# Kernel optimization log

Hardware: AMD Instinct MI355X
Metric: run time of the kernel (lower is better)

Reference implementation:

```python
import jax, jax.numpy as jnp
import numpy as np

N = 80000
E = 1280000
C_IN, HID, C_OUT = 3, 64, 1
DEPTH = 3
KS = [40000, 20000, 10000]  # ceil(0.5 * n) per pooling level
EPS = 1e-5


def gcn_conv(x, W, src, dst, ew, n, fill=2.0):
    # PyG GCNConv with add_self_loops=True; improved => self-loop weight fill=2.0
    h = x @ W                                           # [n, F]
    deg = jax.ops.segment_sum(ew, dst, num_segments=n) + fill
    dinv = jax.lax.rsqrt(deg)
    norm = dinv[src] * ew * dinv[dst]                   # [E]
    agg = jax.ops.segment_sum(norm[:, None] * h[src], dst, num_segments=n)
    return agg + (fill * dinv * dinv)[:, None] * h      # self-loop term


def batchnorm(x, gamma, beta):
    # BatchNorm1d in training mode: biased batch stats over the node dim
    mu = jnp.mean(x, axis=0)
    var = jnp.var(x, axis=0)
    return gamma * (x - mu) * jax.lax.rsqrt(var + EPS) + beta


def gcn_block(x, src, dst, ew, n, W, gamma, beta, fill=2.0):
    return jax.nn.relu(batchnorm(gcn_conv(x, W, src, dst, ew, n, fill), gamma, beta))


def topk_pool(x, src, dst, ew, w, k):
    # TopKPooling with ReLU nonlinearity: score = relu(x.w / ||w||)
    n = x.shape[0]
    score = jax.nn.relu(x @ w / jnp.linalg.norm(w))
    sc, perm = jax.lax.top_k(score, k)
    xk = x[perm] * sc[:, None]
    # filter_adj with fixed edge count: invalid edges get weight 0 (no-op in GCN)
    mapping = jnp.full((n,), -1, dtype=src.dtype).at[perm].set(
        jnp.arange(k, dtype=src.dtype))
    ns, nd = mapping[src], mapping[dst]
    valid = (ns >= 0) & (nd >= 0)
    ns = jnp.where(valid, ns, 0)
    nd = jnp.where(valid, nd, 0)
    new_ew = jnp.where(valid, ew, jnp.zeros((), ew.dtype))
    return xk, ns, nd, new_ew, perm


def _forward(x, edge_index, Wd, gd, bd, pw, Wu, gu, bu, W_out):
    src, dst = edge_index[0], edge_index[1]
    ew = jnp.ones(src.shape, x.dtype)
    n = x.shape[0]
    x = gcn_block(x, src, dst, ew, n, Wd[0], gd[0], bd[0])
    xs, sds, ews, perms = [x], [(src, dst)], [ew], []
    for i in range(DEPTH):
        x, src, dst, ew, perm = topk_pool(x, src, dst, ew, pw[i], KS[i])
        x = gcn_block(x, src, dst, ew, KS[i], Wd[i + 1], gd[i + 1], bd[i + 1])
        if i < DEPTH - 1:
            xs.append(x); sds.append((src, dst)); ews.append(ew)
        perms.append(perm)
    for i in range(DEPTH):
        j = DEPTH - 1 - i
        res = xs[j]; src, dst = sds[j]; ew = ews[j]; perm = perms[j]
        up = jnp.zeros_like(res).at[perm].set(x)
        x = res + up
        if i < DEPTH - 1:
            x = gcn_block(x, src, dst, ew, res.shape[0], Wu[i], gu[i], bu[i])
        else:
            x = jax.nn.sigmoid(
                gcn_conv(x, W_out, src, dst, ew, res.shape[0], fill=1.0))
    return x


def setup_inputs() -> dict:
    key = jax.random.key(0)
    ks = jax.random.split(key, 16)
    nrm = lambda k, shape: jax.random.normal(k, shape, jnp.float32) * 0.1
    inp = {
        "x": jax.random.normal(ks[0], (N, C_IN), jnp.float32),
        "edge_index": jax.random.randint(ks[1], (2, E), 0, N, jnp.int32),
    }
    dims = [(C_IN, HID)] + [(HID, HID)] * DEPTH
    ki = 2
    for l, (a, b) in enumerate(dims):
        inp[f"W_d{l}"] = nrm(ks[ki], (a, b)); ki += 1
        inp[f"g_d{l}"] = jnp.ones((b,), jnp.float32)
        inp[f"b_d{l}"] = jnp.zeros((b,), jnp.float32)
    for l in range(DEPTH):
        inp[f"pw{l}"] = nrm(ks[ki], (HID,)); ki += 1
    for l in range(DEPTH - 1):
        inp[f"W_u{l}"] = nrm(ks[ki], (HID, HID)); ki += 1
        inp[f"g_u{l}"] = jnp.ones((HID,), jnp.float32)
        inp[f"b_u{l}"] = jnp.zeros((HID,), jnp.float32)
    inp["W_out"] = nrm(ks[ki], (HID, C_OUT))
    return inp


def reference(x, edge_index, W_d0, g_d0, b_d0, W_d1, g_d1, b_d1, W_d2, g_d2,
              b_d2, W_d3, g_d3, b_d3, pw0, pw1, pw2, W_u0, g_u0, b_u0,
              W_u1, g_u1, b_u1, W_out):
    Wd = [W_d0, W_d1, W_d2, W_d3]
    gd = [g_d0, g_d1, g_d2, g_d3]
    bd = [b_d0, b_d1, b_d2, b_d3]
    pw = [pw0, pw1, pw2]
    Wu = [W_u0, W_u1]
    gu = [g_u0, g_u1]
    bu = [b_u0, b_u1]
    return _forward(x, edge_index, Wd, gd, bd, pw, Wu, gu, bu, W_out)
```

## Files before the change

kernel.cpp:

```cpp
#include <hip/hip_runtime.h>
#include <cstdint>
#include <utility>

#define NN0 80000
#define NE 1280000
#define MMB_GRID 1024

static inline int cdiv(int a, int b){ return (a+b-1)/b; }

__global__ void k_matmul_bn(const float* __restrict__ x, const float* __restrict__ W,
                            float* __restrict__ h, float* __restrict__ part, int n){
  __shared__ float ls[64], lq[64];
  int f = threadIdx.x & 63;
  float sa = 0.f, sq = 0.f;
  int total = n*64, stride = gridDim.x*blockDim.x;
  for (int t = blockIdx.x*blockDim.x + threadIdx.x; t < total; t += stride){
    int i = t >> 6;
    const float* xr = x + i*64;
    const float* wc = W + f;
    float s = 0.f;
    #pragma unroll
    for (int k2 = 0; k2 < 64; k2++) s += xr[k2]*wc[k2*64];
    h[t] = s; sa += s; sq += s*s;
  }
  if (threadIdx.x < 64){ ls[threadIdx.x] = 0.f; lq[threadIdx.x] = 0.f; }
  __syncthreads();
  atomicAdd(&ls[f], sa); atomicAdd(&lq[f], sq);
  __syncthreads();
  if (threadIdx.x < 128)
    part[blockIdx.x*128 + threadIdx.x] =
      (threadIdx.x < 64) ? ls[threadIdx.x] : lq[threadIdx.x-64];
}

__global__ void k_matmul_bn3(const float* __restrict__ x, const float* __restrict__ W,
                             float* __restrict__ h, float* __restrict__ part, int n){
  __shared__ float ls[64], lq[64];
  int f = threadIdx.x & 63;
  float sa = 0.f, sq = 0.f;
  int total = n*64, stride = gridDim.x*blockDim.x;
  for (int t = blockIdx.x*blockDim.x + threadIdx.x; t < total; t += stride){
    int i = t >> 6;
    float s = x[i*3]*W[f] + x[i*3+1]*W[64+f] + x[i*3+2]*W[128+f];
    h[t] = s; sa += s; sq += s*s;
  }
  if (threadIdx.x < 64){ ls[threadIdx.x] = 0.f; lq[threadIdx.x] = 0.f; }
  __syncthreads();
  atomicAdd(&ls[f], sa); atomicAdd(&lq[f], sq);
  __syncthreads();
  if (threadIdx.x < 128)
    part[blockIdx.x*128 + threadIdx.x] =
      (threadIdx.x < 64) ? ls[threadIdx.x] : lq[threadIdx.x-64];
}

__global__ void k_stats_reduce(const float* __restrict__ part, float* __restrict__ stats){
  int c = blockIdx.x, lane = threadIdx.x;
  float s = 0.f;
  for (int b = lane; b < MMB_GRID; b += 64) s += part[b*128 + c];
  for (int o = 32; o > 0; o >>= 1) s += __shfl_xor(s, o);
  if (lane == 0) stats[c] = s;
}

__global__ void k_matvec(const float* __restrict__ x, const float* __restrict__ W,
                         float* __restrict__ h1, int n){
  int lane = threadIdx.x & 63, w = threadIdx.x >> 6;
  int wid = blockIdx.x*4 + w, nw = gridDim.x*4;
  float wv = W[lane];
  for (int i = wid; i < n; i += nw){
    float v = x[i*64+lane]*wv;
    for (int o = 32; o > 0; o >>= 1) v += __shfl_xor(v, o);
    if (lane == 0) h1[i] = v;
  }
}

__global__ void k_zero_i(int* __restrict__ p, int n){
  int t = blockIdx.x*blockDim.x + threadIdx.x;
  if (t < n) p[t] = 0;
}

__global__ void k_scan_part(const int* __restrict__ in, int* __restrict__ bsum, int n){
  __shared__ int ws[256];
  int base = blockIdx.x*1024 + threadIdx.x*4;
  int s = 0;
  #pragma unroll
  for (int u = 0; u < 4; u++){ int i = base+u; if (i < n) s += in[i]; }
  ws[threadIdx.x] = s; __syncthreads();
  for (int st = 128; st > 0; st >>= 1){
    if (threadIdx.x < st) ws[threadIdx.x] += ws[threadIdx.x+st];
    __syncthreads();
  }
  if (threadIdx.x == 0) bsum[blockIdx.x] = ws[0];
}

__global__ void k_scan_fin_rp(const int* __restrict__ in, const int* __restrict__ bsum, int nb,
                              int* __restrict__ rp, int* __restrict__ cursor, int n){
  __shared__ int bws[256]; __shared__ int ws[256];
  int t = threadIdx.x;
  bws[t] = (t < nb) ? bsum[t] : 0; __syncthreads();
  for (int st = 1; st < 256; st <<= 1){
    int a = (t >= st) ? bws[t-st] : 0; __syncthreads();
    bws[t] += a; __syncthreads();
  }
  int blockoff = (blockIdx.x == 0) ? 0 : bws[blockIdx.x-1];
  int base = blockIdx.x*1024 + t*4;
  int v[4]; int s = 0;
  #pragma unroll
  for (int u = 0; u < 4; u++){ int i = base+u; v[u] = (i < n) ? in[i] : 0; s += v[u]; }
  ws[t] = s; __syncthreads();
  for (int st = 1; st < 256; st <<= 1){
    int a = (t >= st) ? ws[t-st] : 0; __syncthreads();
    ws[t] += a; __syncthreads();
  }
  int off = blockoff + ws[t] - s;
  #pragma unroll
  for (int u = 0; u < 4; u++){
    int i = base+u;
    if (i < n){
      rp[i] = off; cursor[i] = off; off += v[u];
      if (i == n-1) rp[n] = off;
    }
  }
}

__global__ void k_hist_full(const int* __restrict__ dst, int* __restrict__ indeg, int ne){
  int e = blockIdx.x*blockDim.x + threadIdx.x;
  if (e < ne) atomicAdd(&indeg[dst[e]], 1);
}
__global__ void k_scatter_full(const int* __restrict__ src, const int* __restrict__ dst,
                               int* __restrict__ cursor, int* __restrict__ col, int ne){
  int e = blockIdx.x*blockDim.x + threadIdx.x;
  if (e >= ne) return;
  int pos = atomicAdd(&cursor[dst[e]], 1);
  col[pos] = src[e];
}

__global__ void k_hist_mapped(const int* __restrict__ rp_p, const int* __restrict__ col_p,
                              const int* __restrict__ mapv, int* __restrict__ indeg, int np){
  int d = blockIdx.x*blockDim.x + threadIdx.x;
  if (d >= np) return;
  int md = mapv[d];
  if (md < 0) return;
  int c = 0, e = rp_p[d+1];
  for (int j = rp_p[d]; j < e; j++) if (mapv[col_p[j]] >= 0) c++;
  indeg[md] = c;
}
__global__ void k_scatter_mapped(const int* __restrict__ rp_p, const int* __restrict__ col_p,
                                 const int* __restrict__ mapv, const int* __restrict__ rp_c,
                                 int* __restrict__ col_c, int np){
  int d = blockIdx.x*blockDim.x + threadIdx.x;
  if (d >= np) return;
  int md = mapv[d];
  if (md < 0) return;
  int pos = rp_c[md], e = rp_p[d+1];
  for (int j = rp_p[d]; j < e; j++){
    int ms = mapv[col_p[j]];
    if (ms >= 0) col_c[pos++] = ms;
  }
}

__global__ void k_dinv_rp(const int* __restrict__ rp, float* __restrict__ dinv,
                          float fill, int n){
  int i = blockIdx.x*blockDim.x + threadIdx.x;
  if (i < n) dinv[i] = 1.0f/sqrtf((float)(rp[i+1]-rp[i]) + fill);
}

__global__ void k_gather64(const int* __restrict__ rp, const int* __restrict__ col,
                           const float* __restrict__ dinv, const float* __restrict__ x,
                           float* __restrict__ y, int n){
  int t = blockIdx.x*blockDim.x + threadIdx.x;
  int i = t >> 6, f = t & 63;
  if (i >= n) return;
  int beg = rp[i], end = rp[i+1];
  float di = dinv[i];
  float acc = 0.f;
  for (int j = beg; j < end; j++){
    int s = col[j];
    acc += dinv[s]*x[s*64+f];
  }
  y[i*64+f] = di*acc + 2.f*di*di*x[i*64+f];
}

__global__ void k_gather3(const int* __restrict__ rp, const int* __restrict__ col,
                          const float* __restrict__ dinv, const float* __restrict__ x,
                          float* __restrict__ y, int n){
  int i = blockIdx.x*blockDim.x + threadIdx.x;
  if (i >= n) return;
  int beg = rp[i], end = rp[i+1];
  float di = dinv[i];
  float a0 = 0.f, a1 = 0.f, a2 = 0.f;
  for (int j = beg; j < end; j++){
    int s = col[j];
    float ds = dinv[s];
    a0 += ds*x[s*3+0]; a1 += ds*x[s*3+1]; a2 += ds*x[s*3+2];
  }
  float sl = 2.f*di*di;
  y[i*3+0] = di*a0 + sl*x[i*3+0];
  y[i*3+1] = di*a1 + sl*x[i*3+1];
  y[i*3+2] = di*a2 + sl*x[i*3+2];
}

__global__ void k_gather_sig(const int* __restrict__ rp, const int* __restrict__ col,
                             const float* __restrict__ dinv, const float* __restrict__ h1,
                             float* __restrict__ out, int n){
  int i = blockIdx.x*blockDim.x + threadIdx.x;
  if (i >= n) return;
  int beg = rp[i], end = rp[i+1];
  float di = dinv[i];
  float acc = 0.f;
  for (int j = beg; j < end; j++) acc += dinv[col[j]]*h1[col[j]];
  float v = di*acc + di*di*h1[i];
  out[i] = 1.f/(1.f+expf(-v));
}

__global__ void k_bnrelu(float* __restrict__ x, const float* __restrict__ stats,
                         const float* __restrict__ gamma, const float* __restrict__ beta,
                         int n) {
  int t = blockIdx.x*blockDim.x + threadIdx.x;
  if (t >= n*64) return;
  int f = t & 63;
  float inv_n = 1.0f/(float)n;
  float mu = stats[f]*inv_n;
  float var = stats[64+f]*inv_n - mu*mu;
  float v = gamma[f]*(x[t]-mu)*(1.0f/sqrtf(var+1e-5f)) + beta[f];
  x[t] = fmaxf(v, 0.f);
}

__global__ void k_bnrelu_score(float* __restrict__ x, const float* __restrict__ stats,
                               const float* __restrict__ gamma, const float* __restrict__ beta,
                               const float* __restrict__ pw,
                               float* __restrict__ score, unsigned* __restrict__ key,
                               int* __restrict__ idx, int n, int P){
  int lane = threadIdx.x & 63, w = threadIdx.x >> 6;
  int wid = blockIdx.x*4 + w, nw = gridDim.x*4;
  float inv_n = 1.f/(float)n;
  float mu = stats[lane]*inv_n;
  float var = stats[64+lane]*inv_n - mu*mu;
  float gs = gamma[lane]*(1.f/sqrtf(var+1e-5f));
  float bt = beta[lane];
  float pv = pw[lane];
  float q = pv*pv;
  for (int o = 32; o > 0; o >>= 1) q += __shfl_xor(q, o);
  float qn = 1.f/sqrtf(q);
  for (int i = wid; i < n; i += nw){
    float v = fmaxf(gs*(x[i*64+lane]-mu)+bt, 0.f);
    x[i*64+lane] = v;
    float s = v*pv;
    for (int o = 32; o > 0; o >>= 1) s += __shfl_xor(s, o);
    if (lane == 0){
      float sc = fmaxf(s*qn, 0.f);
      score[i] = sc; key[i] = ~__float_as_uint(sc); idx[i] = i;
    }
  }
  for (int g = n + wid; g < P; g += nw)
    if (lane == 0){ key[g] = 0xFFFFFFFFu; idx[g] = 0; }
}

__global__ void k_radix_hist(const unsigned* __restrict__ key, int* __restrict__ hist,
                             int shift, int nblk){
  __shared__ int lh[256];
  lh[threadIdx.x] = 0; __syncthreads();
  int base = blockIdx.x*1024 + threadIdx.x;
  #pragma unroll
  for (int u = 0; u < 4; u++){
    unsigned d = (key[base + u*256] >> shift) & 255u;
    atomicAdd(&lh[d], 1);
  }
  __syncthreads();
  hist[threadIdx.x*nblk + blockIdx.x] = lh[threadIdx.x];
}

__global__ void k_radix_scatter(const unsigned* __restrict__ keyin, const int* __restrict__ idxin,
                                unsigned* __restrict__ keyout, int* __restrict__ idxout,
                                const int* __restrict__ hist, int shift, int nblk){
  __shared__ int dbase[256], run[256], sc[256];
  __shared__ int wcnt[4][256];
  int t = threadIdx.x, lane = t & 63, w = t >> 6;
  int pre = 0, tot = 0;
  for (int b = 0; b < nblk; b++){
    int v = hist[t*nblk + b];
    if (b < blockIdx.x) pre += v;
    tot += v;
  }
  sc[t] = tot; __syncthreads();
  for (int st = 1; st < 256; st <<= 1){
    int a = (t >= st) ? sc[t-st] : 0; __syncthreads();
    sc[t] += a; __syncthreads();
  }
  dbase[t] = sc[t] - tot + pre;
  run[t] = 0;
  for (int u = 0; u < 4; u++){
    wcnt[0][t] = 0; wcnt[1][t] = 0; wcnt[2][t] = 0; wcnt[3][t] = 0;
    __syncthreads();
    int g = blockIdx.x*1024 + u*256 + t;
    unsigned kk = keyin[g]; int id = idxin[g];
    unsigned d = (kk >> shift) & 255u;
    unsigned long long m = ~0ull;
    #pragma unroll
    for (int b = 0; b < 8; b++){
      unsigned long long bal = __ballot((d >> b) & 1u);
      m &= ((d >> b) & 1u) ? bal : ~bal;
    }
    int rnk = __popcll(m & ((1ull << lane) - 1ull));
    if (rnk == 0) wcnt[w][d] = __popcll(m);
    __syncthreads();
    int off2 = run[d] + rnk;
    for (int w2 = 0; w2 < w; w2++) off2 += wcnt[w2][d];
    int pos = dbase[d] + off2;
    keyout[pos] = kk; idxout[pos] = id;
    __syncthreads();
    run[t] += wcnt[0][t] + wcnt[1][t] + wcnt[2][t] + wcnt[3][t];
    __syncthreads();
  }
}

__global__ void k_select_sorted(const int* __restrict__ idxs, int* __restrict__ perm,
                                int* __restrict__ mapping, int n, int k){
  int r = blockIdx.x*blockDim.x + threadIdx.x;
  if (r >= n) return;
  int i = idxs[r];
  mapping[i] = (r < k) ? r : -1;
  if (r < k) perm[r] = i;
}

__global__ void k_gather_scale(const float* __restrict__ x, const float* __restrict__ score,
                               const int* __restrict__ perm, float* __restrict__ xk, int k) {
  int t = blockIdx.x*blockDim.x + threadIdx.x;
  if (t >= k*64) return;
  int r = t >> 6, f = t & 63;
  int i = perm[r];
  xk[t] = x[i*64+f]*score[i];
}

__global__ void k_scatter_add(const float* __restrict__ xup, const int* __restrict__ perm,
                              float* __restrict__ res, int k) {
  int t = blockIdx.x*blockDim.x + threadIdx.x;
  if (t >= k*64) return;
  int r = t >> 6, f = t & 63;
  res[perm[r]*64+f] += xup[t];
}

extern "C" void kernel_launch(void* const* d_in, const int* in_sizes, int n_in,
                              void* d_out, int out_size, void* d_ws, size_t ws_size,
                              hipStream_t stream) {
  const float* x_in = (const float*)d_in[0];
  const int* ei = (const int*)d_in[1];
  const int* src0 = ei;
  const int* dst0 = ei + NE;
  const float* W_d[4] = {(const float*)d_in[2],(const float*)d_in[5],(const float*)d_in[8],(const float*)d_in[11]};
  const float* g_d[4] = {(const float*)d_in[3],(const float*)d_in[6],(const float*)d_in[9],(const float*)d_in[12]};
  const float* b_d[4] = {(const float*)d_in[4],(const float*)d_in[7],(const float*)d_in[10],(const float*)d_in[13]};
  const float* pw[3]  = {(const float*)d_in[14],(const float*)d_in[15],(const float*)d_in[16]};
  const float* W_u[2] = {(const float*)d_in[17],(const float*)d_in[20]};
  const float* g_u[2] = {(const float*)d_in[18],(const float*)d_in[21]};
  const float* b_u[2] = {(const float*)d_in[19],(const float*)d_in[22]};
  const float* W_out  = (const float*)d_in[23];
  float* out = (float*)d_out;

  float* base = (float*)d_ws;
  size_t off = 0;
  auto alloc = [&](size_t nf){ float* p = base + off; off += nf; return p; };
  float* x0 = alloc(5120000);
  float* x1 = alloc(2560000);
  float* x2 = alloc(1280000);
  float* x3 = alloc(640000);
  float* A  = alloc(2560000);
  float* h  = alloc(5120000);
  int* col0 = (int*)alloc(NE);
  int* col1 = (int*)alloc(NE);
  int* col2 = (int*)alloc(NE);
  int* col3 = (int*)alloc(NE);
  int* rp0 = (int*)alloc(80001);
  int* rp1 = (int*)alloc(40001);
  int* rp2 = (int*)alloc(20001);
  int* rp3 = (int*)alloc(10001);
  int* indeg  = (int*)alloc(NN0);
  int* cursor = (int*)alloc(NN0);
  float* dinv0  = alloc(NN0);
  float* dinv0f = alloc(NN0);
  float* dinv1  = alloc(40000);
  float* dinv2  = alloc(20000);
  float* dinv3  = alloc(10000);
  float* score = alloc(NN0);
  int* mapv = (int*)alloc(NN0);
  int* p0 = (int*)alloc(40000);
  int* p1 = (int*)alloc(20000);
  int* p2 = (int*)alloc(10000);
  float* stats = alloc(128);
  float* part  = alloc(MMB_GRID*128);
  unsigned* keyA = (unsigned*)alloc(81920);
  unsigned* keyB = (unsigned*)alloc(81920);
  int* idxA = (int*)alloc(81920);
  int* idxB = (int*)alloc(81920);
  int* hist = (int*)alloc(81920);
  int* bsum = (int*)alloc(256);
  (void)ws_size; (void)in_sizes; (void)n_in; (void)out_size;

  const int B = 256;

  auto scan_csr = [&](const int* indeg_, int* rp, int* cur, int n2){
    int nb = cdiv(n2, 1024);
    k_scan_part  <<<nb, 256, 0, stream>>>(indeg_, bsum, n2);
    k_scan_fin_rp<<<nb, 256, 0, stream>>>(indeg_, bsum, nb, rp, cur, n2);
  };

  auto conv = [&](const float* xin, int Fin, const float* W, int n,
                  const int* rp, const int* col, const float* dv, float* dstb){
    if (Fin == 3){
      k_gather3   <<<cdiv(n,B), B, 0, stream>>>(rp, col, dv, xin, h, n);
      k_matmul_bn3<<<MMB_GRID, B, 0, stream>>>(h, W, dstb, part, n);
    } else {
      k_gather64  <<<cdiv(n*64,B), B, 0, stream>>>(rp, col, dv, xin, h, n);
      k_matmul_bn <<<MMB_GRID, B, 0, stream>>>(h, W, dstb, part, n);
    }
    k_stats_reduce<<<128, 64, 0, stream>>>(part, stats);
  };

  auto pool = [&](float* xb, const float* g, const float* bt, const float* w,
                  int n, int k, int* pm, float* xk){
    int nblk = cdiv(n, 1024), P = nblk*1024;
    k_bnrelu_score<<<512, B, 0, stream>>>(xb, stats, g, bt, w, score, keyA, idxA, n, P);
    unsigned* ka = keyA; int* ia = idxA; unsigned* kb = keyB; int* ib = idxB;
    for (int pass = 0; pass < 4; pass++){
      k_radix_hist   <<<nblk, 256, 0, stream>>>(ka, hist, pass*8, nblk);
      k_radix_scatter<<<nblk, 256, 0, stream>>>(ka, ia, kb, ib, hist, pass*8, nblk);
      std::swap(ka, kb); std::swap(ia, ib);
    }
    k_select_sorted<<<cdiv(n,B), B, 0, stream>>>(ia, pm, mapv, n, k);
    k_gather_scale <<<cdiv(k*64,B), B, 0, stream>>>(xb, score, pm, xk, k);
  };

  auto csr_mapped = [&](const int* rp_p, const int* col_p, int np, int nc,
                        int* rp_c, int* col_c, float* dv){
    k_hist_mapped<<<cdiv(np,B), B, 0, stream>>>(rp_p, col_p, mapv, indeg, np);
    scan_csr(indeg, rp_c, cursor, nc);
    k_scatter_mapped<<<cdiv(np,B), B, 0, stream>>>(rp_p, col_p, mapv, rp_c, col_c, np);
    k_dinv_rp<<<cdiv(nc,B), B, 0, stream>>>(rp_c, dv, 2.f, nc);
  };

  k_zero_i   <<<cdiv(NN0,B), B, 0, stream>>>(indeg, NN0);
  k_hist_full<<<cdiv(NE,B),  B, 0, stream>>>(dst0, indeg, NE);
  scan_csr(indeg, rp0, cursor, NN0);
  k_scatter_full<<<cdiv(NE,B), B, 0, stream>>>(src0, dst0, cursor, col0, NE);
  k_dinv_rp<<<cdiv(NN0,B), B, 0, stream>>>(rp0, dinv0,  2.f, NN0);
  k_dinv_rp<<<cdiv(NN0,B), B, 0, stream>>>(rp0, dinv0f, 1.f, NN0);

  conv(x_in, 3, W_d[0], NN0, rp0, col0, dinv0, x0);
  pool(x0, g_d[0], b_d[0], pw[0], NN0, 40000, p0, A);
  csr_mapped(rp0, col0, NN0, 40000, rp1, col1, dinv1);

  conv(A, 64, W_d[1], 40000, rp1, col1, dinv1, x1);
  pool(x1, g_d[1], b_d[1], pw[1], 40000, 20000, p1, A);
  csr_mapped(rp1, col1, 40000, 20000, rp2, col2, dinv2);

  conv(A, 64, W_d[2], 20000, rp2, col2, dinv2, x2);
  pool(x2, g_d[2], b_d[2], pw[2], 20000, 10000, p2, A);
  csr_mapped(rp2, col2, 20000, 10000, rp3, col3, dinv3);

  conv(A, 64, W_d[3], 10000, rp3, col3, dinv3, x3);
  k_bnrelu<<<cdiv(10000*64,B), B, 0, stream>>>(x3, stats, g_d[3], b_d[3], 10000);

  k_scatter_add<<<cdiv(10000*64,B), B, 0, stream>>>(x3, p2, x2, 10000);
  conv(x2, 64, W_u[0], 20000, rp2, col2, dinv2, A);
  k_bnrelu<<<cdiv(20000*64,B), B, 0, stream>>>(A, stats, g_u[0], b_u[0], 20000);

  k_scatter_add<<<cdiv(20000*64,B), B, 0, stream>>>(A, p1, x1, 20000);
  conv(x1, 64, W_u[1], 40000, rp1, col1, dinv1, A);
  k_bnrelu<<<cdiv(40000*64,B), B, 0, stream>>>(A, stats, g_u[1], b_u[1], 40000);

  k_scatter_add<<<cdiv(40000*64,B), B, 0, stream>>>(A, p0, x0, 40000);

  float* h1 = score;
  k_matvec<<<512, B, 0, stream>>>(x0, W_out, h1, NN0);
  k_gather_sig<<<cdiv(NN0,B), B, 0, stream>>>(rp0, col0, dinv0f, h1, out, NN0);
}
```

Baseline: 899.8 us.

## Build level-0 CSR via stable 3-pass radix sort of edges by destination

Replaces the atomic histogram plus atomic-cursor scatter for the initial CSR with a three-pass 6-bit LSD radix sort of (dst, src) pairs, followed by a binary search per node to find row pointers and both dinv arrays. It also folds dinv computation into the scan kernel for pooled levels and fuses select and gather-scale into one kernel. The aim is to avoid contended global atomics and to produce sorted, deterministic column order that gathers better. In exchange it adds nine extra launches and several full passes over 1.28M edges, plus extra workspace.

```diff
diff --git a/kernel.cpp b/kernel.cpp
--- a/kernel.cpp
+++ b/kernel.cpp
@@ -5,6 +5,8 @@
 #define NN0 80000
 #define NE 1280000
 #define MMB_GRID 1024
+#define EB 2048
+#define ENB 625
 
 static inline int cdiv(int a, int b){ return (a+b-1)/b; }
 
@@ -72,9 +74,65 @@
   }
 }
 
-__global__ void k_zero_i(int* __restrict__ p, int n){
-  int t = blockIdx.x*blockDim.x + threadIdx.x;
-  if (t < n) p[t] = 0;
+__global__ void k_ehist6(const int* __restrict__ key, int* __restrict__ hist, int shift){
+  __shared__ int lh[64];
+  if (threadIdx.x < 64) lh[threadIdx.x] = 0;
+  __syncthreads();
+  int base = blockIdx.x*EB + threadIdx.x;
+  #pragma unroll
+  for (int u = 0; u < 8; u++)
+    atomicAdd(&lh[(key[base + u*256] >> shift) & 63], 1);
+  __syncthreads();
+  if (threadIdx.x < 64) hist[threadIdx.x*ENB + blockIdx.x] = lh[threadIdx.x];
+}
+
+__global__ void k_escatter6(const int* __restrict__ keyin, const int* __restrict__ valin,
+                            int* __restrict__ keyout, int* __restrict__ valout,
+                            const int* __restrict__ hist, int shift){
+  __shared__ int dbase[64], run[64], wcnt[4][64];
+  int t = threadIdx.x, lane = t & 63, w = t >> 6;
+  if (t < 64){ dbase[t] = hist[t*ENB + blockIdx.x]; run[t] = 0; }
+  __syncthreads();
+  for (int u = 0; u < 8; u++){
+    if (t < 64){ wcnt[0][t]=0; wcnt[1][t]=0; wcnt[2][t]=0; wcnt[3][t]=0; }
+    __syncthreads();
+    int g = blockIdx.x*EB + u*256 + t;
+    int kk = keyin[g], vv = valin[g];
+    int d = (kk >> shift) & 63;
+    unsigned long long m = ~0ull;
+    #pragma unroll
+    for (int b = 0; b < 6; b++){
+      unsigned long long bal = __ballot((d >> b) & 1);
+      m &= ((d >> b) & 1) ? bal : ~bal;
+    }
+    int rnk = __popcll(m & ((1ull << lane) - 1ull));
+    if (rnk == 0) wcnt[w][d] = __popcll(m);
+    __syncthreads();
+    int off2 = run[d] + rnk;
+    for (int w2 = 0; w2 < w; w2++) off2 += wcnt[w2][d];
+    int pos = dbase[d] + off2;
+    keyout[pos] = kk; valout[pos] = vv;
+    __syncthreads();
+    if (t < 64) run[t] += wcnt[0][t] + wcnt[1][t] + wcnt[2][t] + wcnt[3][t];
+    __syncthreads();
+  }
+}
+
+__global__ void k_rp_search(const int* __restrict__ skey, int* __restrict__ rp,
+                            float* __restrict__ dinvA, float* __restrict__ dinvB, int n){
+  int i = blockIdx.x*blockDim.x + threadIdx.x;
+  if (i >= n) return;
+  int lo = 0, hi = NE;
+  while (lo < hi){ int mid = (lo+hi)>>1; if (skey[mid] < i) lo = mid+1; else hi = mid; }
+  int a = lo;
+  lo = a; hi = NE;
+  while (lo < hi){ int mid = (lo+hi)>>1; if (skey[mid] < i+1) lo = mid+1; else hi = mid; }
+  int b2 = lo;
+  rp[i] = a;
+  if (i == n-1) rp[n] = NE;
+  float deg = (float)(b2 - a);
+  dinvA[i] = 1.0f/sqrtf(deg + 2.f);
+  dinvB[i] = 1.0f/sqrtf(deg + 1.f);
 }
 
 __global__ void k_scan_part(const int* __restrict__ in, int* __restrict__ bsum, int n){
@@ -92,7 +150,7 @@
 }
 
 __global__ void k_scan_fin_rp(const int* __restrict__ in, const int* __restrict__ bsum, int nb,
-                              int* __restrict__ rp, int* __restrict__ cursor, int n){
+                              int* __restrict__ rp, float* __restrict__ dinvA, int n){
   __shared__ int bws[256]; __shared__ int ws[256];
   int t = threadIdx.x;
   bws[t] = (t < nb) ? bsum[t] : 0; __syncthreads();
@@ -115,22 +173,37 @@
   for (int u = 0; u < 4; u++){
     int i = base+u;
     if (i < n){
-      rp[i] = off; cursor[i] = off; off += v[u];
+      rp[i] = off; off += v[u];
+      dinvA[i] = 1.0f/sqrtf((float)v[u] + 2.f);
       if (i == n-1) rp[n] = off;
     }
   }
 }
 
-__global__ void k_hist_full(const int* __restrict__ dst, int* __restrict__ indeg, int ne){
-  int e = blockIdx.x*blockDim.x + threadIdx.x;
-  if (e < ne) atomicAdd(&indeg[dst[e]], 1);
-}
-__global__ void k_scatter_full(const int* __restrict__ src, const int* __restrict__ dst,
-                               int* __restrict__ cursor, int* __restrict__ col, int ne){
-  int e = blockIdx.x*blockDim.x + threadIdx.x;
-  if (e >= ne) return;
-  int pos = atomicAdd(&cursor[dst[e]], 1);
-  col[pos] = src[e];
+__global__ void k_scan_fin_flat(int* __restrict__ data, const int* __restrict__ bsum, int nb, int n){
+  __shared__ int bws[256]; __shared__ int ws[256];
+  int t = threadIdx.x;
+  bws[t] = (t < nb) ? bsum[t] : 0; __syncthreads();
+  for (int st = 1; st < 256; st <<= 1){
+    int a = (t >= st) ? bws[t-st] : 0; __syncthreads();
+    bws[t] += a; __syncthreads();
+  }
+  int blockoff = (blockIdx.x == 0) ? 0 : bws[blockIdx.x-1];
+  int base = blockIdx.x*1024 + t*4;
+  int v[4]; int s = 0;
+  #pragma unroll
+  for (int u = 0; u < 4; u++){ int i = base+u; v[u] = (i < n) ? data[i] : 0; s += v[u]; }
+  ws[t] = s; __syncthreads();
+  for (int st = 1; st < 256; st <<= 1){
+    int a = (t >= st) ? ws[t-st] : 0; __syncthreads();
+    ws[t] += a; __syncthreads();
+  }
+  int off = blockoff + ws[t] - s;
+  #pragma unroll
+  for (int u = 0; u < 4; u++){
+    int i = base+u;
+    if (i < n){ data[i] = off; off += v[u]; }
+  }
 }
 
 __global__ void k_hist_mapped(const int* __restrict__ rp_p, const int* __restrict__ col_p,
@@ -155,12 +228,6 @@
     int ms = mapv[col_p[j]];
     if (ms >= 0) col_c[pos++] = ms;
   }
-}
-
-__global__ void k_dinv_rp(const int* __restrict__ rp, float* __restrict__ dinv,
-                          float fill, int n){
-  int i = blockIdx.x*blockDim.x + threadIdx.x;
-  if (i < n) dinv[i] = 1.0f/sqrtf((float)(rp[i+1]-rp[i]) + fill);
 }
 
 __global__ void k_gather64(const int* __restrict__ rp, const int* __restrict__ col,
@@ -312,22 +379,20 @@
   }
 }
 
-__global__ void k_select_sorted(const int* __restrict__ idxs, int* __restrict__ perm,
-                                int* __restrict__ mapping, int n, int k){
-  int r = blockIdx.x*blockDim.x + threadIdx.x;
-  if (r >= n) return;
-  int i = idxs[r];
-  mapping[i] = (r < k) ? r : -1;
-  if (r < k) perm[r] = i;
-}
-
-__global__ void k_gather_scale(const float* __restrict__ x, const float* __restrict__ score,
-                               const int* __restrict__ perm, float* __restrict__ xk, int k) {
+__global__ void k_select_gather(const int* __restrict__ idxs, const float* __restrict__ x,
+                                const float* __restrict__ score, int* __restrict__ perm,
+                                int* __restrict__ mapv, float* __restrict__ xk, int n, int k){
   int t = blockIdx.x*blockDim.x + threadIdx.x;
-  if (t >= k*64) return;
-  int r = t >> 6, f = t & 63;
-  int i = perm[r];
-  xk[t] = x[i*64+f]*score[i];
+  if (t < n){
+    int i = idxs[t];
+    mapv[i] = (t < k) ? t : -1;
+    if (t < k) perm[t] = i;
+  }
+  if (t < k*64){
+    int r = t >> 6, f = t & 63;
+    int i = idxs[r];
+    xk[t] = x[i*64+f]*score[i];
+  }
 }
 
 __global__ void k_scatter_add(const float* __restrict__ xup, const int* __restrict__ perm,
@@ -368,12 +433,15 @@
   int* col1 = (int*)alloc(NE);
   int* col2 = (int*)alloc(NE);
   int* col3 = (int*)alloc(NE);
+  int* ek1 = (int*)alloc(NE);
+  int* ev1 = (int*)alloc(NE);
+  int* ek2 = (int*)alloc(NE);
+  int* ev2 = (int*)alloc(NE);
   int* rp0 = (int*)alloc(80001);
   int* rp1 = (int*)alloc(40001);
   int* rp2 = (int*)alloc(20001);
   int* rp3 = (int*)alloc(10001);
   int* indeg  = (int*)alloc(NN0);
-  int* cursor = (int*)alloc(NN0);
   float* dinv0  = alloc(NN0);
   float* dinv0f = alloc(NN0);
   float* dinv1  = alloc(40000);
@@ -391,15 +459,21 @@
   int* idxA = (int*)alloc(81920);
   int* idxB = (int*)alloc(81920);
   int* hist = (int*)alloc(81920);
+  int* ehist = (int*)alloc(64*ENB);
   int* bsum = (int*)alloc(256);
   (void)ws_size; (void)in_sizes; (void)n_in; (void)out_size;
 
   const int B = 256;
 
-  auto scan_csr = [&](const int* indeg_, int* rp, int* cur, int n2){
+  auto scan_flat = [&](int* data, int n2){
+    int nb = cdiv(n2, 1024);
+    k_scan_part    <<<nb, 256, 0, stream>>>(data, bsum, n2);
+    k_scan_fin_flat<<<nb, 256, 0, stream>>>(data, bsum, nb, n2);
+  };
+  auto scan_csr = [&](const int* indeg_, int* rp, float* dv, int n2){
     int nb = cdiv(n2, 1024);
     k_scan_part  <<<nb, 256, 0, stream>>>(indeg_, bsum, n2);
-    k_scan_fin_rp<<<nb, 256, 0, stream>>>(indeg_, bsum, nb, rp, cur, n2);
+    k_scan_fin_rp<<<nb, 256, 0, stream>>>(indeg_, bsum, nb, rp, dv, n2);
   };
 
   auto conv = [&](const float* xin, int Fin, const float* W, int n,
@@ -424,24 +498,26 @@
       k_radix_scatter<<<nblk, 256, 0, stream>>>(ka, ia, kb, ib, hist, pass*8, nblk);
       std::swap(ka, kb); std::swap(ia, ib);
     }
-    k_select_sorted<<<cdiv(n,B), B, 0, stream>>>(ia, pm, mapv, n, k);
-    k_gather_scale <<<cdiv(k*64,B), B, 0, stream>>>(xb, score, pm, xk, k);
+    k_select_gather<<<cdiv(k*64,B), B, 0, stream>>>(ia, xb, score, pm, mapv, xk, n, k);
   };
 
   auto csr_mapped = [&](const int* rp_p, const int* col_p, int np, int nc,
                         int* rp_c, int* col_c, float* dv){
     k_hist_mapped<<<cdiv(np,B), B, 0, stream>>>(rp_p, col_p, mapv, indeg, np);
-    scan_csr(indeg, rp_c, cursor, nc);
+    scan_csr(indeg, rp_c, dv, nc);
     k_scatter_mapped<<<cdiv(np,B), B, 0, stream>>>(rp_p, col_p, mapv, rp_c, col_c, np);
-    k_dinv_rp<<<cdiv(nc,B), B, 0, stream>>>(rp_c, dv, 2.f, nc);
   };
 
-  k_zero_i   <<<cdiv(NN0,B), B, 0, stream>>>(indeg, NN0);
-  k_hist_full<<<cdiv(NE,B),  B, 0, stream>>>(dst0, indeg, NE);
-  scan_csr(indeg, rp0, cursor, NN0);
-  k_scatter_full<<<cdiv(NE,B), B, 0, stream>>>(src0, dst0, cursor, col0, NE);
-  k_dinv_rp<<<cdiv(NN0,B), B, 0, stream>>>(rp0, dinv0,  2.f, NN0);
-  k_dinv_rp<<<cdiv(NN0,B), B, 0, stream>>>(rp0, dinv0f, 1.f, NN0);
+  k_ehist6   <<<ENB, B, 0, stream>>>(dst0, ehist, 0);
+  scan_flat(ehist, 64*ENB);
+  k_escatter6<<<ENB, B, 0, stream>>>(dst0, src0, ek1, ev1, ehist, 0);
+  k_ehist6   <<<ENB, B, 0, stream>>>(ek1, ehist, 6);
+  scan_flat(ehist, 64*ENB);
+  k_escatter6<<<ENB, B, 0, stream>>>(ek1, ev1, ek2, ev2, ehist, 6);
+  k_ehist6   <<<ENB, B, 0, stream>>>(ek2, ehist, 12);
+  scan_flat(ehist, 64*ENB);
+  k_escatter6<<<ENB, B, 0, stream>>>(ek2, ev2, ek1, col0, ehist, 12);
+  k_rp_search<<<cdiv(NN0,B), B, 0, stream>>>(ek1, rp0, dinv0, dinv0f, NN0);
 
   conv(x_in, 3, W_d[0], NN0, rp0, col0, dinv0, x0);
   pool(x0, g_d[0], b_d[0], pw[0], NN0, 40000, p0, A);
```

After: 809.0 us. 1.11x faster.
